# Kernel tuning notes

Measured on AMD Instinct MI355X. Metric: run time of the kernel, lower is better.

The kernel has to match this reference:

```python
import jax, jax.numpy as jnp
import numpy as np

L, D, H, V, TB = 4, 768, 12, 50257, 2048  # n_layer, n_embd, n_head, vocab, block_size


def setup_inputs() -> dict:
    key = jax.random.key(0)
    ks = jax.random.split(key, 12)
    s = 0.02
    def n(k, shape):
        return jax.random.normal(k, shape, jnp.float32) * s
    return dict(
        idx=jax.random.randint(ks[0], (1, 2048), 0, V),
        targets=jax.random.randint(ks[1], (1, 2048), 0, V),
        wte=n(ks[2], (V, D)),
        wpe=n(ks[3], (TB, D)),
        ln1_w=jnp.ones((L, D)), ln1_b=jnp.zeros((L, D)),
        attn_w=n(ks[4], (L, D, 3 * D)), attn_b=jnp.zeros((L, 3 * D)),
        attn_proj_w=n(ks[5], (L, D, D)), attn_proj_b=jnp.zeros((L, D)),
        ln2_w=jnp.ones((L, D)), ln2_b=jnp.zeros((L, D)),
        fc_w=n(ks[6], (L, D, 4 * D)), fc_b=jnp.zeros((L, 4 * D)),
        mlp_proj_w=n(ks[7], (L, 4 * D, D)), mlp_proj_b=jnp.zeros((L, D)),
        lnf_w=jnp.ones((D,)), lnf_b=jnp.zeros((D,)),
        head_w=n(ks[8], (D, V)), head_b=jnp.zeros((V,)),
    )


def _ln(x, w, b, eps=1e-5):
    m = x.mean(-1, keepdims=True)
    v = ((x - m) ** 2).mean(-1, keepdims=True)
    return (x - m) * jax.lax.rsqrt(v + eps) * w + b


def reference(idx, targets, wte, wpe, ln1_w, ln1_b, attn_w, attn_b,
              attn_proj_w, attn_proj_b, ln2_w, ln2_b, fc_w, fc_b,
              mlp_proj_w, mlp_proj_b, lnf_w, lnf_b, head_w, head_b):
    B, T = idx.shape
    Dh = D // H
    x = wte[idx] + wpe[:T]  # [B,T,D]
    mask = jnp.tril(jnp.ones((T, T), bool))
    neg = jnp.finfo(x.dtype).min
    scale = jnp.asarray(1.0 / np.sqrt(Dh), x.dtype)
    for i in range(L):
        h = _ln(x, ln1_w[i], ln1_b[i])
        qkv = h @ attn_w[i] + attn_b[i]
        q, k, v = jnp.split(qkv, 3, axis=-1)
        q = q.reshape(B, T, H, Dh).transpose(0, 2, 1, 3)
        k = k.reshape(B, T, H, Dh).transpose(0, 2, 1, 3)
        v = v.reshape(B, T, H, Dh).transpose(0, 2, 1, 3)
        scores = jnp.einsum('bhqd,bhkd->bhqk', q, k) * scale
        scores = jnp.where(mask, scores, neg)  # causal masked_fill
        attn = jax.nn.softmax(scores, axis=-1)
        o = jnp.einsum('bhqk,bhkd->bhqd', attn, v)
        o = o.transpose(0, 2, 1, 3).reshape(B, T, D)
        x = x + o @ attn_proj_w[i] + attn_proj_b[i]
        h = _ln(x, ln2_w[i], ln2_b[i])
        h = jax.nn.gelu(h @ fc_w[i] + fc_b[i], approximate=True)  # tanh GELU
        x = x + h @ mlp_proj_w[i] + mlp_proj_b[i]
    x = _ln(x, lnf_w, lnf_b)
    logits = x @ head_w + head_b  # [B,T,V]
    logp = jax.nn.log_softmax(logits, axis=-1)
    nll = -jnp.take_along_axis(logp, targets[..., None], axis=-1).squeeze(-1)
    loss = nll.mean()
    return logits, loss
```

## Files before the change

kernel.cpp:

```cpp
#include <hip/hip_runtime.h>
#include <hip/hip_bf16.h>
#include <math.h>

using bf16   = __hip_bfloat16;
using f32x4  = __attribute__((ext_vector_type(4))) float;
using bf16x8 = __attribute__((ext_vector_type(8))) short;
using s16x4  = __attribute__((ext_vector_type(4))) short;

constexpr int SEQ    = 2048;
constexpr int DMODEL = 768;
constexpr int NHEAD  = 12;
constexpr int NV     = 50257;
constexpr int NVPAD  = 50304;
constexpr int NB     = NVPAD / 128;
constexpr int NLAYER = 4;
constexpr int KSPLIT = 3;

__device__ __forceinline__ void gload_lds16(const void* g, void* s) {
    __builtin_amdgcn_global_load_lds((const __attribute__((address_space(1))) void*)g,
                                     (__attribute__((address_space(3))) void*)s, 16, 0, 0);
}

__global__ __launch_bounds__(192) void embed_kernel(const int* __restrict__ idx,
                                                    const float* __restrict__ wte,
                                                    const float* __restrict__ wpe,
                                                    float* __restrict__ x) {
    int t = blockIdx.x;
    int tok = idx[t];
    const float4* a = (const float4*)(wte + (size_t)tok * DMODEL);
    const float4* b = (const float4*)(wpe + (size_t)t * DMODEL);
    float4* o = (float4*)(x + (size_t)t * DMODEL);
    int d = threadIdx.x;
    float4 u = a[d], v = b[d];
    u.x += v.x; u.y += v.y; u.z += v.z; u.w += v.w;
    o[d] = u;
}

__global__ __launch_bounds__(256) void ln_kernel(const float* __restrict__ x,
                                                 const float* __restrict__ w,
                                                 const float* __restrict__ b,
                                                 bf16* __restrict__ out) {
    __shared__ float red[8];
    int row = blockIdx.x, tid = threadIdx.x;
    const float* xr = x + (size_t)row * DMODEL;
    float v[3];
    float s = 0.f, ss = 0.f;
#pragma unroll
    for (int j = 0; j < 3; j++) {
        v[j] = xr[tid + j * 256];
        s += v[j];
        ss += v[j] * v[j];
    }
#pragma unroll
    for (int off = 32; off; off >>= 1) {
        s  += __shfl_down(s,  off, 64);
        ss += __shfl_down(ss, off, 64);
    }
    int wid = tid >> 6, lane = tid & 63;
    if (lane == 0) { red[wid] = s; red[4 + wid] = ss; }
    __syncthreads();
    s  = red[0] + red[1] + red[2] + red[3];
    ss = red[4] + red[5] + red[6] + red[7];
    float mean = s * (1.0f / DMODEL);
    float var  = ss * (1.0f / DMODEL) - mean * mean;
    float rstd = rsqrtf(var + 1e-5f);
#pragma unroll
    for (int j = 0; j < 3; j++) {
        int d = tid + j * 256;
        out[(size_t)row * DMODEL + d] = __float2bfloat16((v[j] - mean) * rstd * w[d] + b[d]);
    }
}

__global__ __launch_bounds__(192) void kredln_kernel(const float* __restrict__ partial,
                                                     const float* __restrict__ gbias,
                                                     float* __restrict__ x,
                                                     const float* __restrict__ lnw,
                                                     const float* __restrict__ lnb,
                                                     bf16* __restrict__ h) {
    __shared__ float red[6];
    int row = blockIdx.x, t = threadIdx.x;
    size_t off = (size_t)row * DMODEL + t * 4;
    f32x4 v = *(f32x4*)&x[off];
    float4 b = *(const float4*)&gbias[t * 4];
    v[0] += b.x; v[1] += b.y; v[2] += b.z; v[3] += b.w;
#pragma unroll
    for (int z = 0; z < KSPLIT; z++) {
        f32x4 p = *(const f32x4*)&partial[(size_t)z * SEQ * DMODEL + off];
        v[0] += p[0]; v[1] += p[1]; v[2] += p[2]; v[3] += p[3];
    }
    *(f32x4*)&x[off] = v;
    float s  = v[0] + v[1] + v[2] + v[3];
    float ss = v[0] * v[0] + v[1] * v[1] + v[2] * v[2] + v[3] * v[3];
#pragma unroll
    for (int o2 = 32; o2; o2 >>= 1) {
        s  += __shfl_down(s,  o2, 64);
        ss += __shfl_down(ss, o2, 64);
    }
    int wid = t >> 6, lane = t & 63;
    if (lane == 0) { red[wid] = s; red[3 + wid] = ss; }
    __syncthreads();
    s  = red[0] + red[1] + red[2];
    ss = red[3] + red[4] + red[5];
    float mean = s * (1.0f / DMODEL);
    float var  = ss * (1.0f / DMODEL) - mean * mean;
    float rstd = rsqrtf(var + 1e-5f);
    float4 w4 = *(const float4*)&lnw[t * 4];
    float4 b4 = *(const float4*)&lnb[t * 4];
    s16x4 pk;
    {
        bf16 t0 = __float2bfloat16((v[0] - mean) * rstd * w4.x + b4.x);
        bf16 t1 = __float2bfloat16((v[1] - mean) * rstd * w4.y + b4.y);
        bf16 t2 = __float2bfloat16((v[2] - mean) * rstd * w4.z + b4.z);
        bf16 t3 = __float2bfloat16((v[3] - mean) * rstd * w4.w + b4.w);
        pk[0] = *reinterpret_cast<short*>(&t0);
        pk[1] = *reinterpret_cast<short*>(&t1);
        pk[2] = *reinterpret_cast<short*>(&t2);
        pk[3] = *reinterpret_cast<short*>(&t3);
    }
    *(s16x4*)&h[off] = pk;
}

__global__ __launch_bounds__(256) void transpb_kernel(const float* __restrict__ W,
                                                      bf16* __restrict__ Wt,
                                                      int K, int N,
                                                      size_t wstride, size_t tstride) {
    __shared__ float t[64][65];
    int l = blockIdx.z;
    W  += (size_t)l * wstride;
    Wt += (size_t)l * tstride;
    int n0 = blockIdx.x << 6, k0 = blockIdx.y << 6;
    int tid = threadIdx.x;
#pragma unroll
    for (int i = 0; i < 16; i++) {
        int id = tid + (i << 8);
        int r = id >> 6, c = id & 63;
        int n = n0 + c;
        t[r][c] = (n < N) ? W[(size_t)(k0 + r) * N + n] : 0.0f;
    }
    __syncthreads();
#pragma unroll
    for (int i = 0; i < 16; i++) {
        int id = tid + (i << 8);
        int nr = id >> 6, kc = id & 63;
        Wt[(size_t)(n0 + nr) * K + k0 + kc] = __float2bfloat16(t[kc][nr]);
    }
}

template <int ACT, int RES, int OBF>
__global__ __launch_bounds__(256) void mgemm_kernel(const short* __restrict__ A,
                                                    const short* __restrict__ Wt,
                                                    const float* __restrict__ bias,
                                                    const float* __restrict__ res,
                                                    float* __restrict__ outf,
                                                    bf16* __restrict__ outb,
                                                    int N, int K) {
    __shared__ short As[2][4096];
    __shared__ short Bs[2][4096];
    int tid = threadIdx.x, lane = tid & 63, wid = tid >> 6;
    int bm = blockIdx.y << 7, bn = blockIdx.x << 7;
    int wr = (wid >> 1) << 6, wc = (wid & 1) << 6;
    f32x4 acc[4][4] = {};
    int rA = tid >> 2, sA = tid & 3;
    int q = lane >> 4, rr = lane & 15;

    auto STAGE = [&](int b, int k0) {
#pragma unroll
        for (int i = 0; i < 2; i++) {
            int r = rA + (i << 6);
            int gc = k0 + ((sA ^ ((r >> 1) & 3)) << 3);
            char* dstA = (char*)As + b * 8192 + (i << 12) + (wid << 10);
            char* dstB = (char*)Bs + b * 8192 + (i << 12) + (wid << 10);
            gload_lds16(A  + (size_t)(bm + r) * K + gc, dstA);
            gload_lds16(Wt + (size_t)(bn + r) * K + gc, dstB);
        }
    };

    STAGE(0, 0);
    int cur = 0;
    for (int k0 = 0; k0 < K; k0 += 32) {
        if (k0 + 32 < K) {
            STAGE(cur ^ 1, k0 + 32);
            asm volatile("s_waitcnt vmcnt(4)" ::: "memory");
        } else {
            asm volatile("s_waitcnt vmcnt(0)" ::: "memory");
        }
        __builtin_amdgcn_s_barrier();
        __builtin_amdgcn_sched_barrier(0);
        bf16x8 af[4], bfr[4];
#pragma unroll
        for (int m = 0; m < 4; m++) {
            int rowa = wr + (m << 4) + rr;
            af[m]  = *(const bf16x8*)((const char*)As + cur * 8192 + rowa * 64 + ((q ^ ((rowa >> 1) & 3)) << 4));
            int rowb = wc + (m << 4) + rr;
            bfr[m] = *(const bf16x8*)((const char*)Bs + cur * 8192 + rowb * 64 + ((q ^ ((rowb >> 1) & 3)) << 4));
        }
#pragma unroll
        for (int m = 0; m < 4; m++)
#pragma unroll
            for (int n = 0; n < 4; n++)
                acc[m][n] = __builtin_amdgcn_mfma_f32_16x16x32_bf16(bfr[n], af[m], acc[m][n], 0, 0, 0);
        __builtin_amdgcn_sched_barrier(0);
        __builtin_amdgcn_s_barrier();
        cur ^= 1;
    }

    int cl = lane & 15, g = lane >> 4;
#pragma unroll
    for (int m = 0; m < 4; m++) {
        int row = bm + wr + (m << 4) + cl;
#pragma unroll
        for (int n = 0; n < 4; n++) {
            int col0 = bn + wc + (n << 4) + (g << 2);
            float4 bv = *(const float4*)&bias[col0];
            f32x4 v = acc[m][n];
            v[0] += bv.x; v[1] += bv.y; v[2] += bv.z; v[3] += bv.w;
            if (RES) {
                float4 rv = *(const float4*)&res[(size_t)row * N + col0];
                v[0] += rv.x; v[1] += rv.y; v[2] += rv.z; v[3] += rv.w;
            }
            if (ACT) {
#pragma unroll
                for (int j = 0; j < 4; j++)
                    v[j] = v[j] / (1.0f + __expf(-1.5957691216057308f * (v[j] + 0.044715f * v[j] * v[j] * v[j])));
            }
            if (OBF) {
                s16x4 pk;
#pragma unroll
                for (int j = 0; j < 4; j++) {
                    bf16 t = __float2bfloat16(v[j]);
                    pk[j] = *reinterpret_cast<short*>(&t);
                }
                *(s16x4*)&outb[(size_t)row * N + col0] = pk;
            } else {
                *(f32x4*)&outf[(size_t)row * N + col0] = v;
            }
        }
    }
}

__global__ __launch_bounds__(256) void mgemmp_kernel(const short* __restrict__ A,
                                                     const short* __restrict__ Wt,
                                                     float* __restrict__ partial,
                                                     int N, int Kc, int Kstride) {
    __shared__ short As[2][4096];
    __shared__ short Bs[2][4096];
    int tid = threadIdx.x, lane = tid & 63, wid = tid >> 6;
    int bm = blockIdx.y << 7, bn = blockIdx.x << 7;
    int z = blockIdx.z;
    const short* Ab  = A  + (size_t)z * Kc;
    const short* Wb  = Wt + (size_t)z * Kc;
    int wr = (wid >> 1) << 6, wc = (wid & 1) << 6;
    f32x4 acc[4][4] = {};
    int rA = tid >> 2, sA = tid & 3;
    int q = lane >> 4, rr = lane & 15;

    auto STAGE = [&](int b, int k0) {
#pragma unroll
        for (int i = 0; i < 2; i++) {
            int r = rA + (i << 6);
            int gc = k0 + ((sA ^ ((r >> 1) & 3)) << 3);
            char* dstA = (char*)As + b * 8192 + (i << 12) + (wid << 10);
            char* dstB = (char*)Bs + b * 8192 + (i << 12) + (wid << 10);
            gload_lds16(Ab + (size_t)(bm + r) * Kstride + gc, dstA);
            gload_lds16(Wb + (size_t)(bn + r) * Kstride + gc, dstB);
        }
    };

    STAGE(0, 0);
    int cur = 0;
    for (int k0 = 0; k0 < Kc; k0 += 32) {
        if (k0 + 32 < Kc) {
            STAGE(cur ^ 1, k0 + 32);
            asm volatile("s_waitcnt vmcnt(4)" ::: "memory");
        } else {
            asm volatile("s_waitcnt vmcnt(0)" ::: "memory");
        }
        __builtin_amdgcn_s_barrier();
        __builtin_amdgcn_sched_barrier(0);
        bf16x8 af[4], bfr[4];
#pragma unroll
        for (int m = 0; m < 4; m++) {
            int rowa = wr + (m << 4) + rr;
            af[m]  = *(const bf16x8*)((const char*)As + cur * 8192 + rowa * 64 + ((q ^ ((rowa >> 1) & 3)) << 4));
            int rowb = wc + (m << 4) + rr;
            bfr[m] = *(const bf16x8*)((const char*)Bs + cur * 8192 + rowb * 64 + ((q ^ ((rowb >> 1) & 3)) << 4));
        }
#pragma unroll
        for (int m = 0; m < 4; m++)
#pragma unroll
            for (int n = 0; n < 4; n++)
                acc[m][n] = __builtin_amdgcn_mfma_f32_16x16x32_bf16(bfr[n], af[m], acc[m][n], 0, 0, 0);
        __builtin_amdgcn_sched_barrier(0);
        __builtin_amdgcn_s_barrier();
        cur ^= 1;
    }

    float* outz = partial + (size_t)z * SEQ * DMODEL;
    int cl = lane & 15, g = lane >> 4;
#pragma unroll
    for (int m = 0; m < 4; m++) {
        int row = bm + wr + (m << 4) + cl;
#pragma unroll
        for (int n = 0; n < 4; n++) {
            int col0 = bn + wc + (n << 4) + (g << 2);
            *(f32x4*)&outz[(size_t)row * N + col0] = acc[m][n];
        }
    }
}

__global__ __launch_bounds__(256) void head_kernel(const short* __restrict__ A,
                                                   const short* __restrict__ Wt,
                                                   const float* __restrict__ bias,
                                                   float* __restrict__ out,
                                                   float* __restrict__ pm,
                                                   float* __restrict__ ps) {
    __shared__ short As[4096];
    __shared__ short Bs[4096];
    __shared__ float lm[128][2];
    __shared__ float lsum[128][2];
    constexpr int K = DMODEL;
    int bid = blockIdx.x;
    int swz = (bid & 7) * (6288 / 8) + (bid >> 3);
    int bm = (swz & 15) << 7;
    int bxp = swz >> 4;
    int bn = bxp << 7;
    int tid = threadIdx.x, lane = tid & 63, wid = tid >> 6;
    int wr = (wid >> 1) << 6;
    int wc = (wid & 1) << 6;
    f32x4 acc[4][4] = {};
    int rA = tid >> 2, sA = tid & 3;
    int q = lane >> 4, rr = lane & 15;

    for (int k0 = 0; k0 < K; k0 += 32) {
#pragma unroll
        for (int i = 0; i < 2; i++) {
            int r = rA + (i << 6);
            int gc = k0 + ((sA ^ ((r >> 1) & 3)) << 3);
            char* dstA = (char*)As + (i << 12) + (wid << 10);
            char* dstB = (char*)Bs + (i << 12) + (wid << 10);
            gload_lds16(A  + (size_t)(bm + r) * K + gc, dstA);
            gload_lds16(Wt + (size_t)(bn + r) * K + gc, dstB);
        }
        __syncthreads();
        bf16x8 af[4], bfr[4];
#pragma unroll
        for (int m = 0; m < 4; m++) {
            int rowa = wr + (m << 4) + rr;
            af[m]  = *(const bf16x8*)((const char*)As + rowa * 64 + ((q ^ ((rowa >> 1) & 3)) << 4));
            int rowb = wc + (m << 4) + rr;
            bfr[m] = *(const bf16x8*)((const char*)Bs + rowb * 64 + ((q ^ ((rowb >> 1) & 3)) << 4));
        }
#pragma unroll
        for (int m = 0; m < 4; m++)
#pragma unroll
            for (int n = 0; n < 4; n++)
                acc[m][n] = __builtin_amdgcn_mfma_f32_16x16x32_bf16(bfr[n], af[m], acc[m][n], 0, 0, 0);
        __syncthreads();
    }

    int cl = lane & 15, g = lane >> 4;
#pragma unroll
    for (int m = 0; m < 4; m++) {
        int row = bm + wr + (m << 4) + cl;
#pragma unroll
        for (int n = 0; n < 4; n++) {
            int col0 = bn + wc + (n << 4) + (g << 2);
            f32x4 v = acc[m][n];
            if (col0 + 3 < NV) {
                float4 bv = *(const float4*)&bias[col0];
                v[0] += bv.x; v[1] += bv.y; v[2] += bv.z; v[3] += bv.w;
                *(f32x4*)&out[(size_t)row * NV + col0] = v;
            } else {
#pragma unroll
                for (int j = 0; j < 4; j++) {
                    if (col0 + j < NV) {
                        v[j] += bias[col0 + j];
                        out[(size_t)row * NV + col0 + j] = v[j];
                    } else {
                        v[j] = -1e30f;
                    }
                }
            }
            acc[m][n] = v;
        }
    }
#pragma unroll
    for (int m = 0; m < 4; m++) {
        float t = -1e30f;
#pragma unroll
        for (int n = 0; n < 4; n++)
#pragma unroll
            for (int j = 0; j < 4; j++) t = fmaxf(t, acc[m][n][j]);
        t = fmaxf(t, __shfl_xor(t, 16, 64));
        t = fmaxf(t, __shfl_xor(t, 32, 64));
        if (g == 0) lm[wr + (m << 4) + cl][wid & 1] = t;
    }
    __syncthreads();
#pragma unroll
    for (int m = 0; m < 4; m++) {
        int r = wr + (m << 4) + cl;
        float M = fmaxf(lm[r][0], lm[r][1]);
        float s = 0.f;
#pragma unroll
        for (int n = 0; n < 4; n++)
#pragma unroll
            for (int j = 0; j < 4; j++) s += __expf(acc[m][n][j] - M);
        s += __shfl_xor(s, 16, 64);
        s += __shfl_xor(s, 32, 64);
        if (g == 0) lsum[r][wid & 1] = s;
    }
    __syncthreads();
    if (tid < 128) {
        int r = tid;
        pm[(size_t)(bm + r) * NB + bxp] = fmaxf(lm[r][0], lm[r][1]);
        ps[(size_t)(bm + r) * NB + bxp] = lsum[r][0] + lsum[r][1];
    }
}

__global__ __launch_bounds__(256) void lsered_kernel(const float* __restrict__ pm,
                                                     const float* __restrict__ ps,
                                                     float* __restrict__ lse) {
    int row = (blockIdx.x << 2) + (threadIdx.x >> 6);
    int lane = threadIdx.x & 63;
    const float* pmr = pm + (size_t)row * NB;
    const float* psr = ps + (size_t)row * NB;
    float m = -1e30f, s = 0.f;
    for (int j = lane; j < NB; j += 64) {
        float mb = pmr[j], sb = psr[j];
        float M = fmaxf(m, mb);
        s = s * __expf(m - M) + sb * __expf(mb - M);
        m = M;
    }
#pragma unroll
    for (int off = 32; off; off >>= 1) {
        float m2 = __shfl_xor(m, off, 64), s2 = __shfl_xor(s, off, 64);
        float M = fmaxf(m, m2);
        s = s * __expf(m - M) + s2 * __expf(m2 - M);
        m = M;
    }
    if (lane == 0) lse[row] = m + logf(s);
}

__global__ __launch_bounds__(256) void attn_kernel(const short* __restrict__ qkv,
                                                   bf16* __restrict__ o) {
    __shared__ short Ks[8192];
    __shared__ short Vt[8192];
    __shared__ short Ps[8192];
    int qt = gridDim.x - 1 - blockIdx.x;
    int h = blockIdx.y, tid = threadIdx.x;
    int lane = tid & 63, w = tid >> 6;
    int g = lane >> 4, c = lane & 15;
    int q0 = qt << 6;
    int nkt = (qt >> 1) + 1;

    bf16x8 qa[2];
    {
        const short* src = qkv + (size_t)(q0 + w * 16 + c) * 2304 + h * 64 + g * 8;
        qa[0] = *(const bf16x8*)src;
        qa[1] = *(const bf16x8*)(src + 32);
    }
    float l_i[4] = {};
    f32x4 oacc[4] = {};

    for (int kt = 0; kt < nkt; kt++) {
        __syncthreads();
#pragma unroll
        for (int i = 0; i < 4; i++) {
            int r = (tid >> 3) + i * 32;
            int gslot = (tid & 7) ^ ((r & 7) ^ ((r >> 3) & 7));
            gload_lds16(qkv + (size_t)(kt * 128 + r) * 2304 + 768 + h * 64 + gslot * 8,
                        (char*)Ks + tid * 16 + i * 4096);
        }
#pragma unroll
        for (int ci = 0; ci < 4; ci++) {
            int rv = (tid >> 3) + ci * 32;
            bf16x8 vv = *(const bf16x8*)(qkv + (size_t)(kt * 128 + rv) * 2304 + 1536 + h * 64 + (tid & 7) * 8);
            int slot = rv >> 3;
#pragma unroll
            for (int j = 0; j < 8; j++) {
                int row = (tid & 7) * 8 + j;
                int sp = slot ^ ((row & 7) ^ ((row >> 3) & 7));
                Vt[row * 128 + sp * 8 + (rv & 7)] = vv[j];
            }
        }
        __syncthreads();

        f32x4 sacc[8] = {};
#pragma unroll
        for (int n = 0; n < 8; n++) {
#pragma unroll
            for (int ks = 0; ks < 2; ks++) {
                int row = n * 16 + c;
                int sp = (ks * 4 + g) ^ ((row & 7) ^ ((row >> 3) & 7));
                bf16x8 kf = *(const bf16x8*)(Ks + row * 64 + sp * 8);
                sacc[n] = __builtin_amdgcn_mfma_f32_16x16x32_bf16(qa[ks], kf, sacc[n], 0, 0, 0);
            }
        }
#pragma unroll
        for (int n = 0; n < 8; n++)
#pragma unroll
            for (int i = 0; i < 4; i++) {
                float v = sacc[n][i] * 0.125f;
                if (kt == nkt - 1 && (kt * 128 + n * 16 + c > q0 + w * 16 + g * 4 + i)) v = -1e30f;
                sacc[n][i] = v;
            }
#pragma unroll
        for (int i = 0; i < 4; i++) {
            float rs = 0.f;
            int row = g * 4 + i;
            int sw = (row & 7) ^ (row >> 3);
#pragma unroll
            for (int n = 0; n < 8; n++) {
                float p = __expf(sacc[n][i]);
                rs += p;
                int sp = (2 * n + (c >> 3)) ^ sw;
                bf16 pb = __float2bfloat16(p);
                Ps[w * 2048 + row * 128 + sp * 8 + (c & 7)] = *reinterpret_cast<short*>(&pb);
            }
            rs += __shfl_xor(rs, 1, 16);
            rs += __shfl_xor(rs, 2, 16);
            rs += __shfl_xor(rs, 4, 16);
            rs += __shfl_xor(rs, 8, 16);
            l_i[i] += rs;
        }
        bf16x8 pa[4];
#pragma unroll
        for (int ks = 0; ks < 4; ks++) {
            int sw = (c & 7) ^ (c >> 3);
            int sp = (ks * 4 + g) ^ sw;
            pa[ks] = *(const bf16x8*)(Ps + w * 2048 + c * 128 + sp * 8);
        }
#pragma unroll
        for (int n = 0; n < 4; n++) {
#pragma unroll
            for (int ks = 0; ks < 4; ks++) {
                int row = n * 16 + c;
                int sp = (ks * 4 + g) ^ ((row & 7) ^ ((row >> 3) & 7));
                bf16x8 vf = *(const bf16x8*)(Vt + row * 128 + sp * 8);
                oacc[n] = __builtin_amdgcn_mfma_f32_16x16x32_bf16(pa[ks], vf, oacc[n], 0, 0, 0);
            }
        }
    }
#pragma unroll
    for (int i = 0; i < 4; i++) {
        float inv = 1.0f / l_i[i];
#pragma unroll
        for (int n = 0; n < 4; n++)
            o[(size_t)(q0 + w * 16 + g * 4 + i) * DMODEL + h * 64 + n * 16 + c] =
                __float2bfloat16(oacc[n][i] * inv);
    }
}

__global__ __launch_bounds__(256) void loss_kernel(const float* __restrict__ logits,
                                                   const float* __restrict__ lse,
                                                   const int* __restrict__ targets,
                                                   float* __restrict__ out) {
    __shared__ float red[4];
    int tid = threadIdx.x;
    float acc = 0.f;
    for (int t = tid; t < SEQ; t += 256)
        acc += lse[t] - logits[(size_t)t * NV + targets[t]];
#pragma unroll
    for (int off = 32; off; off >>= 1) acc += __shfl_down(acc, off, 64);
    int wid = tid >> 6, lane = tid & 63;
    if (lane == 0) red[wid] = acc;
    __syncthreads();
    if (tid == 0) out[0] = (red[0] + red[1] + red[2] + red[3]) * (1.0f / SEQ);
}

extern "C" void kernel_launch(void* const* d_in, const int* in_sizes, int n_in,
                              void* d_out, int out_size, void* d_ws, size_t ws_size,
                              hipStream_t stream) {
    const int*   idx         = (const int*)d_in[0];
    const int*   targets     = (const int*)d_in[1];
    const float* wte         = (const float*)d_in[2];
    const float* wpe         = (const float*)d_in[3];
    const float* ln1_w       = (const float*)d_in[4];
    const float* ln1_b       = (const float*)d_in[5];
    const float* attn_w      = (const float*)d_in[6];
    const float* attn_b      = (const float*)d_in[7];
    const float* attn_proj_w = (const float*)d_in[8];
    const float* attn_proj_b = (const float*)d_in[9];
    const float* ln2_w       = (const float*)d_in[10];
    const float* ln2_b       = (const float*)d_in[11];
    const float* fc_w        = (const float*)d_in[12];
    const float* fc_b        = (const float*)d_in[13];
    const float* mlp_proj_w  = (const float*)d_in[14];
    const float* mlp_proj_b  = (const float*)d_in[15];
    const float* lnf_w       = (const float*)d_in[16];
    const float* lnf_b       = (const float*)d_in[17];
    const float* head_w      = (const float*)d_in[18];
    const float* head_b      = (const float*)d_in[19];

    float* logits = (float*)d_out;
    float* loss   = logits + (size_t)SEQ * NV;

    char* p = (char*)d_ws;
    float* x    = (float*)p;  p += (size_t)SEQ * DMODEL * 4;
    bf16*  h    = (bf16*)p;   p += (size_t)SEQ * DMODEL * 2;
    bf16*  o    = (bf16*)p;   p += (size_t)SEQ * DMODEL * 2;
    bf16*  qkvb = (bf16*)p;   p += (size_t)SEQ * 2304 * 2;
    bf16*  fcb  = (bf16*)p;   p += (size_t)SEQ * 3072 * 2;
    float* lse  = (float*)p;  p += (size_t)SEQ * 4;
    float* pm   = (float*)p;  p += (size_t)SEQ * NB * 4;
    float* ps   = (float*)p;  p += (size_t)SEQ * NB * 4;
    bf16*  Wt   = (bf16*)p;

    bf16* wtA = Wt;
    bf16* wtP = wtA + (size_t)4 * 2304 * 768;
    bf16* wtF = wtP + (size_t)4 * 768 * 768;
    bf16* wtM = wtF + (size_t)4 * 3072 * 768;
    float* kscr = (float*)(wtM + (size_t)4 * 768 * 3072);

    embed_kernel<<<SEQ, 192, 0, stream>>>(idx, wte, wpe, x);

    transpb_kernel<<<dim3(2304 / 64, DMODEL / 64, 4), 256, 0, stream>>>(
        attn_w, wtA, DMODEL, 2304, (size_t)DMODEL * 2304, (size_t)2304 * DMODEL);
    transpb_kernel<<<dim3(DMODEL / 64, DMODEL / 64, 4), 256, 0, stream>>>(
        attn_proj_w, wtP, DMODEL, DMODEL, (size_t)DMODEL * DMODEL, (size_t)DMODEL * DMODEL);
    transpb_kernel<<<dim3(3072 / 64, DMODEL / 64, 4), 256, 0, stream>>>(
        fc_w, wtF, DMODEL, 3072, (size_t)DMODEL * 3072, (size_t)3072 * DMODEL);
    transpb_kernel<<<dim3(DMODEL / 64, 3072 / 64, 4), 256, 0, stream>>>(
        mlp_proj_w, wtM, 3072, DMODEL, (size_t)3072 * DMODEL, (size_t)DMODEL * 3072);

    ln_kernel<<<SEQ, 256, 0, stream>>>(x, ln1_w, ln1_b, h);
    for (int l = 0; l < NLAYER; l++) {
        mgemm_kernel<0, 0, 1><<<dim3(2304 / 128, SEQ / 128), 256, 0, stream>>>(
            (const short*)h, (const short*)(wtA + (size_t)l * 2304 * DMODEL),
            attn_b + l * 2304, nullptr, nullptr, qkvb, 2304, DMODEL);
        attn_kernel<<<dim3(SEQ / 64, NHEAD), 256, 0, stream>>>((const short*)qkvb, o);
        mgemmp_kernel<<<dim3(DMODEL / 128, SEQ / 128, KSPLIT), 256, 0, stream>>>(
            (const short*)o, (const short*)(wtP + (size_t)l * DMODEL * DMODEL),
            kscr, DMODEL, DMODEL / KSPLIT, DMODEL);
        kredln_kernel<<<SEQ, 192, 0, stream>>>(
            kscr, attn_proj_b + l * DMODEL, x, ln2_w + l * DMODEL, ln2_b + l * DMODEL, h);
        mgemm_kernel<1, 0, 1><<<dim3(3072 / 128, SEQ / 128), 256, 0, stream>>>(
            (const short*)h, (const short*)(wtF + (size_t)l * 3072 * DMODEL),
            fc_b + l * 3072, nullptr, nullptr, fcb, 3072, DMODEL);
        mgemmp_kernel<<<dim3(DMODEL / 128, SEQ / 128, KSPLIT), 256, 0, stream>>>(
            (const short*)fcb, (const short*)(wtM + (size_t)l * DMODEL * 3072),
            kscr, DMODEL, 3072 / KSPLIT, 3072);
        const float* nw = (l == NLAYER - 1) ? lnf_w : ln1_w + (l + 1) * DMODEL;
        const float* nb = (l == NLAYER - 1) ? lnf_b : ln1_b + (l + 1) * DMODEL;
        kredln_kernel<<<SEQ, 192, 0, stream>>>(
            kscr, mlp_proj_b + l * DMODEL, x, nw, nb, h);
    }

    transpb_kernel<<<dim3(NVPAD / 64, DMODEL / 64, 1), 256, 0, stream>>>(
        head_w, Wt, DMODEL, NV, 0, 0);
    head_kernel<<<dim3(NB * 16), 256, 0, stream>>>(
        (const short*)h, (const short*)Wt, head_b, logits, pm, ps);
    lsered_kernel<<<SEQ / 4, 256, 0, stream>>>(pm, ps, lse);
    loss_kernel<<<1, 256, 0, stream>>>(logits, lse, targets, loss);
}
```

Measured before the change: 1.099 ms.

## Swizzle GEMM block order across XCDs and enlarge LM-head tile to 256 rows

Measured after the change: 1.088 ms. About the same (-1.0%).

```diff
diff --git a/kernel.cpp b/kernel.cpp
--- a/kernel.cpp
+++ b/kernel.cpp
@@ -157,7 +157,11 @@
     __shared__ short As[2][4096];
     __shared__ short Bs[2][4096];
     int tid = threadIdx.x, lane = tid & 63, wid = tid >> 6;
-    int bm = blockIdx.y << 7, bn = blockIdx.x << 7;
+    int bid = blockIdx.x;
+    int chunk = (N >> 7) << 1;
+    int swz = (bid & 7) * chunk + (bid >> 3);
+    int bn = (swz >> 4) << 7;
+    int bm = (swz & 15) << 7;
     int wr = (wid >> 1) << 6, wc = (wid & 1) << 6;
     f32x4 acc[4][4] = {};
     int rA = tid >> 2, sA = tid & 3;
@@ -245,8 +249,14 @@
     __shared__ short As[2][4096];
     __shared__ short Bs[2][4096];
     int tid = threadIdx.x, lane = tid & 63, wid = tid >> 6;
-    int bm = blockIdx.y << 7, bn = blockIdx.x << 7;
-    int z = blockIdx.z;
+    int bid = blockIdx.x;
+    int per_z = (N >> 7) << 4;
+    int chunk = (per_z * KSPLIT) >> 3;
+    int swz = (bid & 7) * chunk + (bid >> 3);
+    int z = swz / per_z;
+    int rem = swz - z * per_z;
+    int bn = (rem >> 4) << 7;
+    int bm = (rem & 15) << 7;
     const short* Ab  = A  + (size_t)z * Kc;
     const short* Wb  = Wt + (size_t)z * Kc;
     int wr = (wid >> 1) << 6, wc = (wid & 1) << 6;
@@ -308,21 +318,21 @@
     }
 }
 
-__global__ __launch_bounds__(256) void head_kernel(const short* __restrict__ A,
+__global__ __launch_bounds__(512) void head_kernel(const short* __restrict__ A,
                                                    const short* __restrict__ Wt,
                                                    const float* __restrict__ bias,
                                                    float* __restrict__ out,
                                                    float* __restrict__ pm,
                                                    float* __restrict__ ps) {
-    __shared__ short As[4096];
+    __shared__ short As[8192];
     __shared__ short Bs[4096];
-    __shared__ float lm[128][2];
-    __shared__ float lsum[128][2];
+    __shared__ float lm[256][2];
+    __shared__ float lsum[256][2];
     constexpr int K = DMODEL;
     int bid = blockIdx.x;
-    int swz = (bid & 7) * (6288 / 8) + (bid >> 3);
-    int bm = (swz & 15) << 7;
-    int bxp = swz >> 4;
+    int swz = (bid & 7) * 393 + (bid >> 3);
+    int bm = (swz & 7) << 8;
+    int bxp = swz >> 3;
     int bn = bxp << 7;
     int tid = threadIdx.x, lane = tid & 63, wid = tid >> 6;
     int wr = (wid >> 1) << 6;
@@ -334,12 +344,13 @@
     for (int k0 = 0; k0 < K; k0 += 32) {
 #pragma unroll
         for (int i = 0; i < 2; i++) {
-            int r = rA + (i << 6);
+            int r = rA + (i << 7);
             int gc = k0 + ((sA ^ ((r >> 1) & 3)) << 3);
-            char* dstA = (char*)As + (i << 12) + (wid << 10);
-            char* dstB = (char*)Bs + (i << 12) + (wid << 10);
-            gload_lds16(A  + (size_t)(bm + r) * K + gc, dstA);
-            gload_lds16(Wt + (size_t)(bn + r) * K + gc, dstB);
+            gload_lds16(A + (size_t)(bm + r) * K + gc, (char*)As + (i << 13) + tid * 16);
+        }
+        {
+            int gc = k0 + ((sA ^ ((rA >> 1) & 3)) << 3);
+            gload_lds16(Wt + (size_t)(bn + rA) * K + gc, (char*)Bs + tid * 16);
         }
         __syncthreads();
         bf16x8 af[4], bfr[4];
@@ -410,7 +421,7 @@
         if (g == 0) lsum[r][wid & 1] = s;
     }
     __syncthreads();
-    if (tid < 128) {
+    if (tid < 256) {
         int r = tid;
         pm[(size_t)(bm + r) * NB + bxp] = fmaxf(lm[r][0], lm[r][1]);
         ps[(size_t)(bm + r) * NB + bxp] = lsum[r][0] + lsum[r][1];
@@ -625,19 +636,19 @@
 
     ln_kernel<<<SEQ, 256, 0, stream>>>(x, ln1_w, ln1_b, h);
     for (int l = 0; l < NLAYER; l++) {
-        mgemm_kernel<0, 0, 1><<<dim3(2304 / 128, SEQ / 128), 256, 0, stream>>>(
+        mgemm_kernel<0, 0, 1><<<dim3((2304 / 128) * 16), 256, 0, stream>>>(
             (const short*)h, (const short*)(wtA + (size_t)l * 2304 * DMODEL),
             attn_b + l * 2304, nullptr, nullptr, qkvb, 2304, DMODEL);
         attn_kernel<<<dim3(SEQ / 64, NHEAD), 256, 0, stream>>>((const short*)qkvb, o);
-        mgemmp_kernel<<<dim3(DMODEL / 128, SEQ / 128, KSPLIT), 256, 0, stream>>>(
+        mgemmp_kernel<<<dim3((DMODEL / 128) * 16 * KSPLIT), 256, 0, stream>>>(
             (const short*)o, (const short*)(wtP + (size_t)l * DMODEL * DMODEL),
             kscr, DMODEL, DMODEL / KSPLIT, DMODEL);
         kredln_kernel<<<SEQ, 192, 0, stream>>>(
             kscr, attn_proj_b + l * DMODEL, x, ln2_w + l * DMODEL, ln2_b + l * DMODEL, h);
-        mgemm_kernel<1, 0, 1><<<dim3(3072 / 128, SEQ / 128), 256, 0, stream>>>(
+        mgemm_kernel<1, 0, 1><<<dim3((3072 / 128) * 16), 256, 0, stream>>>(
             (const short*)h, (const short*)(wtF + (size_t)l * 3072 * DMODEL),
             fc_b + l * 3072, nullptr, nullptr, fcb, 3072, DMODEL);
-        mgemmp_kernel<<<dim3(DMODEL / 128, SEQ / 128, KSPLIT), 256, 0, stream>>>(
+        mgemmp_kernel<<<dim3((DMODEL / 128) * 16 * KSPLIT), 256, 0, stream>>>(
             (const short*)fcb, (const short*)(wtM + (size_t)l * DMODEL * 3072),
             kscr, DMODEL, 3072 / KSPLIT, 3072);
         const float* nw = (l == NLAYER - 1) ? lnf_w : ln1_w + (l + 1) * DMODEL;
@@ -648,7 +659,7 @@
 
     transpb_kernel<<<dim3(NVPAD / 64, DMODEL / 64, 1), 256, 0, stream>>>(
         head_w, Wt, DMODEL, NV, 0, 0);
-    head_kernel<<<dim3(NB * 16), 256, 0, stream>>>(
+    head_kernel<<<dim3(8 * 393), 512, 0, stream>>>(
         (const short*)h, (const short*)Wt, head_b, logits, pm, ps);
     lsered_kernel<<<SEQ / 4, 256, 0, stream>>>(pm, ps, lse);
     loss_kernel<<<1, 256, 0, stream>>>(logits, lse, targets, loss);
```
